# Optimization experiments

Measured on AMD Instinct MI355X. Metric: run time of the kernel, lower is better.

Reference implementation:

```python
import jax, jax.numpy as jnp
import numpy as np

# --- fixed module hyperparameters (from init_kwargs) ---
B, N, DIM = 1, 1024, 1024
HEADS, KV_HEADS, DH = 16, 4, 64
BS = 32                 # block_size
NUM_SEL = 8             # num_selected_blocks (< num blocks, so min() is NUM_SEL)
MEM = 1                 # num_compressed_mem_kv
W = N // BS             # num compress blocks (seq divisible by block -> no padding paths)
G = HEADS // KV_HEADS   # grouped queries per kv head
CDIM = BS * DH          # compress mlp input dim
HID = CDIM              # compress_mlp_expand_factor = 1.0
EPS = 1e-6


def setup_inputs() -> dict:
    key = jax.random.key(0)
    ks = jax.random.split(key, 12)
    s = 0.02
    f32 = jnp.float32
    return {
        "inp": jax.random.normal(ks[0], (B, N, DIM), f32),
        "g_norm": jnp.ones((DIM,), f32),                                   # RMSNorm weight
        "w_qkv": jax.random.normal(ks[1], (DIM, (HEADS + 2 * KV_HEADS) * DH), f32) * s,
        "mem_kv": jax.random.normal(ks[2], (2, KV_HEADS, MEM, DH), f32) * s,
        "k_pos": jax.random.normal(ks[3], (KV_HEADS, BS, DH), f32) * s,    # intra-block pos
        "v_pos": jax.random.normal(ks[4], (KV_HEADS, BS, DH), f32) * s,
        "k_w1": jax.random.normal(ks[5], (CDIM, HID), f32) * s,
        "k_b1": jnp.zeros((HID,), f32),
        "k_w2": jax.random.normal(ks[6], (HID, DH), f32) * s,
        "k_b2": jnp.zeros((DH,), f32),
        "v_w1": jax.random.normal(ks[7], (CDIM, HID), f32) * s,
        "v_b1": jnp.zeros((HID,), f32),
        "v_w2": jax.random.normal(ks[8], (HID, DH), f32) * s,
        "v_b2": jnp.zeros((DH,), f32),
        "gate_w": jax.random.normal(ks[9], (DIM, 2 * HEADS), f32) * s,
        "gate_b": jnp.full((2 * HEADS,), -2.0, f32),                       # bias init from source
        "w_out": jax.random.normal(ks[10], (HEADS * DH, DIM), f32) * s,
    }


def _rotary(x):
    # interleaved rotary (rotary-embedding-torch default), x: (b, h, n, d)
    n, d = x.shape[-2], x.shape[-1]
    inv_freq = 1.0 / (10000.0 ** (jnp.arange(0, d, 2, dtype=jnp.float32) / d))
    freqs = jnp.arange(n, dtype=jnp.float32)[:, None] * inv_freq            # (n, d/2)
    cos = jnp.repeat(jnp.cos(freqs), 2, axis=-1).astype(x.dtype)
    sin = jnp.repeat(jnp.sin(freqs), 2, axis=-1).astype(x.dtype)
    xr = jnp.stack([-x[..., 1::2], x[..., 0::2]], axis=-1).reshape(x.shape)  # rotate_half
    return x * cos + xr * sin


def reference(inp, g_norm, w_qkv, mem_kv, k_pos, v_pos,
              k_w1, k_b1, k_w2, k_b2, v_w1, v_b1, v_w2, v_b2,
              gate_w, gate_b, w_out):
    scale = DH ** -0.5
    # RMSNorm
    x = inp * jax.lax.rsqrt(jnp.mean(jnp.square(inp), -1, keepdims=True) + EPS) * g_norm
    qkv = x @ w_qkv
    q = qkv[..., : HEADS * DH].reshape(B, N, HEADS, DH).transpose(0, 2, 1, 3)
    k = qkv[..., HEADS * DH : (HEADS + KV_HEADS) * DH].reshape(B, N, KV_HEADS, DH).transpose(0, 2, 1, 3)
    v = qkv[..., (HEADS + KV_HEADS) * DH :].reshape(B, N, KV_HEADS, DH).transpose(0, 2, 1, 3)

    # --- compressed branch: MLP-pool each block of BS keys/values ---
    kpe = k + jnp.tile(k_pos, (1, W, 1))[None]               # (B,KV,N,DH)
    vpe = v + jnp.tile(v_pos, (1, W, 1))[None]
    ck = jax.nn.relu(kpe.reshape(B, KV_HEADS, W, CDIM) @ k_w1 + k_b1) @ k_w2 + k_b2   # (B,KV,W,DH)
    cv = jax.nn.relu(vpe.reshape(B, KV_HEADS, W, CDIM) @ v_w1 + v_b1) @ v_w2 + v_b2
    ck = jnp.concatenate([jnp.broadcast_to(mem_kv[0], (B, KV_HEADS, MEM, DH)), ck], axis=2)
    cv = jnp.concatenate([jnp.broadcast_to(mem_kv[1], (B, KV_HEADS, MEM, DH)), cv], axis=2)

    qg = q.reshape(B, KV_HEADS, G, N, DH)
    csim = jnp.einsum('bhgid,bhjd->bhgij', qg, ck) * scale   # (B,KV,G,N,MEM+W)
    cattn = jax.nn.softmax(csim, axis=-1)
    c_out = jnp.einsum('bhgij,bhjd->bhgid', cattn, cv).reshape(B, HEADS, N, DH)

    # rotary only for the fine branch (applied after compressed attention)
    q = _rotary(q)
    k = _rotary(k)

    # --- block selection from compressed similarities (query heads share) ---
    imp = csim[..., MEM:].mean(axis=2)                       # (B,KV,N,W)
    imp = jnp.pad(imp, ((0, 0), (0, 0), (0, 0), (1, 0)), constant_values=-1000.0)
    imp = jax.nn.softmax(imp, axis=-1)[..., 1:]
    sel_vals, sel_idx = jax.lax.top_k(imp, NUM_SEL)          # (B,KV,N,S)
    fmask = sel_vals > 1e-10

    # always include each query's own block (diagonal block), fully attended
    own = jnp.broadcast_to((jnp.arange(N) // BS)[None, None, :, None], (B, KV_HEADS, N, 1))
    sel_idx = jnp.concatenate([sel_idx, own], axis=-1)       # (B,KV,N,S+1)
    fmask = jnp.concatenate([fmask, jnp.ones(own.shape, bool)], axis=-1)

    # --- gather selected KV blocks per query position (irregular access) ---
    kb = k.reshape(B, KV_HEADS, W, BS, DH)
    vb = v.reshape(B, KV_HEADS, W, BS, DH)
    b_ix = jnp.arange(B)[:, None, None, None]
    h_ix = jnp.arange(KV_HEADS)[None, :, None, None]
    J = (NUM_SEL + 1) * BS
    fk = kb[b_ix, h_ix, sel_idx].reshape(B, KV_HEADS, N, J, DH)
    fv = vb[b_ix, h_ix, sel_idx].reshape(B, KV_HEADS, N, J, DH)
    fmask = jnp.repeat(fmask, BS, axis=-1)                   # (B,KV,N,J)

    fq = q.reshape(B, KV_HEADS, G, N, DH)
    fsim = jnp.einsum('bhgid,bhijd->bhgij', fq, fk) * scale  # (B,KV,G,N,J)
    fsim = jnp.where(fmask[:, :, None], fsim, -jnp.finfo(fsim.dtype).max)
    fattn = jax.nn.softmax(fsim, axis=-1)
    f_out = jnp.einsum('bhgij,bhijd->bhgid', fattn, fv).reshape(B, HEADS, N, DH)

    # --- learned sigmoid gating of the two branches ---
    gates = jax.nn.sigmoid(x @ gate_w + gate_b).reshape(B, N, HEADS, 2).transpose(0, 2, 1, 3)
    out = gates[..., 0:1] * c_out + gates[..., 1:2] * f_out  # (B,H,N,DH)
    out = out.transpose(0, 2, 1, 3).reshape(B, N, HEADS * DH)
    return out @ w_out
```

## Files before the change

### kernel.cpp

```cpp
#include <hip/hip_runtime.h>
#include <math.h>

#define NTOK 1024
#define DDIM 1024
#define HEADS 16
#define KVH 4
#define DH 64
#define BSZ 32
#define NSEL 8
#define WBLK 32
#define GQ 4
#define CDIM 2048
#define HIDN 2048
#define QKVD 1536
#define SCALE 0.125f
#define NEGINF (-__builtin_inff())

typedef unsigned short u16;
typedef u16   u16x8  __attribute__((ext_vector_type(8)));
typedef short short8 __attribute__((ext_vector_type(8)));
typedef float f32x4  __attribute__((ext_vector_type(4)));

__device__ __forceinline__ u16 f2bf(float f) {
    unsigned u = __float_as_uint(f);
    return (u16)((u + 0x7fffu + ((u >> 16) & 1u)) >> 16);
}
__device__ __forceinline__ float bf2f(u16 h) { return __uint_as_float(((unsigned)h) << 16); }

__device__ __forceinline__ void glds16(const void* g, void* l) {
    __builtin_amdgcn_global_load_lds(
        (const __attribute__((address_space(1))) unsigned int*)g,
        (__attribute__((address_space(3))) unsigned int*)l, 16, 0, 0);
}

__device__ __forceinline__ size_t tiled_off(int row, int k, int K) {
    return ((size_t)((row >> 4) * (K >> 5) + (k >> 5)) * 64 +
            ((row & 15) | (((k >> 3) & 3) << 4))) * 8;
}

__global__ void rmsnorm_kernel(const float* __restrict__ inp, const float* __restrict__ g,
                               u16* __restrict__ xhi, u16* __restrict__ xlo) {
    int t = threadIdx.x;
    int half = t >> 7, tid = t & 127;
    int n = blockIdx.x * 2 + half;
    const float4* row = (const float4*)(inp + (size_t)n * DDIM);
    float4 v0 = row[tid * 2], v1 = row[tid * 2 + 1];
    float ss = v0.x*v0.x + v0.y*v0.y + v0.z*v0.z + v0.w*v0.w
             + v1.x*v1.x + v1.y*v1.y + v1.z*v1.z + v1.w*v1.w;
    for (int off = 32; off; off >>= 1) ss += __shfl_down(ss, off);
    __shared__ float red[4];
    if ((t & 63) == 0) red[t >> 6] = ss;
    __syncthreads();
    float tot = red[half * 2] + red[half * 2 + 1];
    float r = 1.f / sqrtf(tot * (1.f / DDIM) + 1e-6f);
    const float4* gp = (const float4*)g;
    float4 g0 = gp[tid * 2], g1 = gp[tid * 2 + 1];
    float o[8] = { v0.x*r*g0.x, v0.y*r*g0.y, v0.z*r*g0.z, v0.w*r*g0.w,
                   v1.x*r*g1.x, v1.y*r*g1.y, v1.z*r*g1.z, v1.w*r*g1.w };
    u16x8 h, l;
#pragma unroll
    for (int i = 0; i < 8; ++i) {
        u16 hh = f2bf(o[i]);
        h[i] = hh;
        l[i] = f2bf(o[i] - bf2f(hh));
    }
    size_t ob = tiled_off(n, tid * 8, DDIM);
    *(u16x8*)&xhi[ob] = h;
    *(u16x8*)&xlo[ob] = l;
}

__global__ void transpose_split(const float* __restrict__ W, u16* __restrict__ Thi,
                                u16* __restrict__ Tlo, int K, int N) {
    __shared__ float tile[64][65];
    int k0 = blockIdx.y * 64, n0 = blockIdx.x * 64;
    int t = threadIdx.x;
    int r = t >> 4, c4 = (t & 15) * 4;
#pragma unroll
    for (int p = 0; p < 4; ++p) {
        float4 v = *(const float4*)&W[(size_t)(k0 + r + p * 16) * N + n0 + c4];
        tile[r + p * 16][c4 + 0] = v.x;
        tile[r + p * 16][c4 + 1] = v.y;
        tile[r + p * 16][c4 + 2] = v.z;
        tile[r + p * 16][c4 + 3] = v.w;
    }
    __syncthreads();
    int n = t >> 2, ks = (t & 3) * 16;
#pragma unroll
    for (int c = 0; c < 2; ++c) {
        u16x8 h, l;
#pragma unroll
        for (int j = 0; j < 8; ++j) {
            float v = tile[ks + c * 8 + j][n];
            u16 hh = f2bf(v);
            h[j] = hh;
            l[j] = f2bf(v - bf2f(hh));
        }
        size_t ob = tiled_off(n0 + n, k0 + ks + c * 8, K);
        *(u16x8*)&Thi[ob] = h;
        if (Tlo) *(u16x8*)&Tlo[ob] = l;
    }
}

__global__ void pad_small_tiled(const float* __restrict__ W, const float* __restrict__ b,
                                u16* __restrict__ Thi, u16* __restrict__ Tlo,
                                float* __restrict__ bias_pad, int K, int Xn, int KLOG) {
    int idx = blockIdx.x * 256 + threadIdx.x;
    int k = (idx & ((K >> 3) - 1)) * 8;
    int n = idx >> (KLOG - 3);
    if (n >= 128) return;
    u16x8 h, l;
#pragma unroll
    for (int j = 0; j < 8; ++j) {
        float v = (n < Xn) ? W[(size_t)(k + j) * Xn + n] : 0.f;
        u16 hh = f2bf(v);
        h[j] = hh;
        l[j] = f2bf(v - bf2f(hh));
    }
    size_t ob = tiled_off(n, k, K);
    *(u16x8*)&Thi[ob] = h;
    *(u16x8*)&Tlo[ob] = l;
    if (k == 0) bias_pad[n] = (n < Xn) ? b[n] : 0.f;
}

template<int SPLIT, int ACT, int FINAL>
__global__ __launch_bounds__(256, 1)
void gemm_tiled(const u16* __restrict__ Ahi0, const u16* __restrict__ Alo0,
                const u16* __restrict__ Bhi0, const u16* __restrict__ Blo0,
                const float* __restrict__ bias0, float* __restrict__ C0,
                const u16* __restrict__ Ahi1, const u16* __restrict__ Alo1,
                const u16* __restrict__ Bhi1, const u16* __restrict__ Blo1,
                const float* __restrict__ bias1, float* __restrict__ C1,
                int M, int N, int K, int S) {
    int batch = blockIdx.z / S;
    int s = blockIdx.z - batch * S;
    const u16* Ahi = batch ? Ahi1 : Ahi0;
    const u16* Alo = batch ? Alo1 : Alo0;
    const u16* Bhi = batch ? Bhi1 : Bhi0;
    const u16* Blo = batch ? Blo1 : Blo0;
    const float* bias = batch ? bias1 : bias0;
    float* C = batch ? C1 : C0;

    constexpr int PARTS = (SPLIT == 3) ? 2 : 1;
    __shared__ u16 smA[2 * PARTS * 8 * 512];
    __shared__ u16 smB[2 * PARTS * 8 * 512];

    int tid = threadIdx.x;
    int w = tid >> 6, L = tid & 63;
    int m15 = L & 15, q = L >> 4;
    int KT = K >> 5;
    int rowTile = blockIdx.y * 8, colTile = blockIdx.x * 8;
    int NIT = (K / S) >> 5;
    int kb0 = s * NIT;
    int aw = w & 1, bw = w >> 1;

    f32x4 acc[4][4];
#pragma unroll
    for (int i = 0; i < 4; ++i)
#pragma unroll
        for (int j = 0; j < 4; ++j) acc[i][j] = (f32x4){0.f, 0.f, 0.f, 0.f};

    auto stage = [&](int buf, int kb) {
#pragma unroll
        for (int rl = 0; rl < 2; ++rl) {
            int rb = 2 * w + rl;
            glds16(Ahi + ((size_t)(rowTile + rb) * KT + kb) * 512 + (size_t)L * 8,
                   &smA[((buf * PARTS + 0) * 8 + rb) * 512]);
            glds16(Bhi + ((size_t)(colTile + rb) * KT + kb) * 512 + (size_t)L * 8,
                   &smB[((buf * PARTS + 0) * 8 + rb) * 512]);
            if constexpr (SPLIT == 3) {
                glds16(Alo + ((size_t)(rowTile + rb) * KT + kb) * 512 + (size_t)L * 8,
                       &smA[((buf * PARTS + 1) * 8 + rb) * 512]);
                glds16(Blo + ((size_t)(colTile + rb) * KT + kb) * 512 + (size_t)L * 8,
                       &smB[((buf * PARTS + 1) * 8 + rb) * 512]);
            }
        }
    };

    stage(0, kb0);
    for (int it = 0; it < NIT; ++it) {
        __syncthreads();
        if (it + 1 < NIT) stage((it + 1) & 1, kb0 + it + 1);
        int buf = it & 1;
        short8 ah[4], bh[4];
#pragma unroll
        for (int i = 0; i < 4; ++i) {
            ah[i] = *(const short8*)&smA[((buf * PARTS + 0) * 8 + aw * 4 + i) * 512 + L * 8];
            bh[i] = *(const short8*)&smB[((buf * PARTS + 0) * 8 + bw * 4 + i) * 512 + L * 8];
        }
        if constexpr (SPLIT == 3) {
            short8 al[4], bl[4];
#pragma unroll
            for (int i = 0; i < 4; ++i) {
                al[i] = *(const short8*)&smA[((buf * PARTS + 1) * 8 + aw * 4 + i) * 512 + L * 8];
                bl[i] = *(const short8*)&smB[((buf * PARTS + 1) * 8 + bw * 4 + i) * 512 + L * 8];
            }
#pragma unroll
            for (int i = 0; i < 4; ++i)
#pragma unroll
                for (int j = 0; j < 4; ++j) {
                    acc[i][j] = __builtin_amdgcn_mfma_f32_16x16x32_bf16(ah[i], bl[j], acc[i][j], 0, 0, 0);
                    acc[i][j] = __builtin_amdgcn_mfma_f32_16x16x32_bf16(al[i], bh[j], acc[i][j], 0, 0, 0);
                    acc[i][j] = __builtin_amdgcn_mfma_f32_16x16x32_bf16(ah[i], bh[j], acc[i][j], 0, 0, 0);
                }
        } else {
#pragma unroll
            for (int i = 0; i < 4; ++i)
#pragma unroll
                for (int j = 0; j < 4; ++j)
                    acc[i][j] = __builtin_amdgcn_mfma_f32_16x16x32_bf16(ah[i], bh[j], acc[i][j], 0, 0, 0);
        }
    }

    if constexpr (FINAL == 0) C += (size_t)s * M * N;
#pragma unroll
    for (int i = 0; i < 4; ++i) {
        int row = rowTile * 16 + aw * 64 + i * 16 + q * 4;
#pragma unroll
        for (int j = 0; j < 4; ++j) {
            int col = colTile * 16 + bw * 64 + j * 16 + m15;
            float bv = (FINAL && bias) ? bias[col] : 0.f;
#pragma unroll
            for (int r = 0; r < 4; ++r) {
                float v = acc[i][j][r];
                if constexpr (FINAL) {
                    v += bv;
                    if (ACT == 1) v = fmaxf(v, 0.f);
                    if (ACT == 2) v = 1.f / (1.f + expf(-v));
                }
                C[(size_t)(row + r) * N + col] = v;
            }
        }
    }
}

template<int ACT>
__global__ void reduce_f32(const float* __restrict__ P0, const float* __restrict__ bias0,
                           float* __restrict__ C0,
                           const float* __restrict__ P1, const float* __restrict__ bias1,
                           float* __restrict__ C1, int S, int M, int N) {
    const float* P = blockIdx.y ? P1 : P0;
    const float* bias = blockIdx.y ? bias1 : bias0;
    float* C = blockIdx.y ? C1 : C0;
    int idx = blockIdx.x * 256 + threadIdx.x;
    int mn4 = (M * N) >> 2;
    if (idx >= mn4) return;
    f32x4 a = ((const f32x4*)P)[idx];
    for (int s = 1; s < S; ++s) a += ((const f32x4*)P)[(size_t)s * mn4 + idx];
    int col = (idx % (N >> 2)) * 4;
    f32x4 o;
#pragma unroll
    for (int j = 0; j < 4; ++j) {
        float v = a[j] + (bias ? bias[col + j] : 0.f);
        if (ACT == 1) v = fmaxf(v, 0.f);
        if (ACT == 2) v = 1.f / (1.f + expf(-v));
        o[j] = v;
    }
    ((f32x4*)C)[idx] = o;
}

__global__ void reduce_hid(const float* __restrict__ P0, const float* __restrict__ b0,
                           u16* __restrict__ hi0, u16* __restrict__ lo0,
                           const float* __restrict__ P1, const float* __restrict__ b1,
                           u16* __restrict__ hi1, u16* __restrict__ lo1, int S) {
    const float* P = blockIdx.y ? P1 : P0;
    const float* bias = blockIdx.y ? b1 : b0;
    u16* hi = blockIdx.y ? hi1 : hi0;
    u16* lo = blockIdx.y ? lo1 : lo0;
    int idx = blockIdx.x * 256 + threadIdx.x;
    int col = (idx & 255) * 8, rowi = idx >> 8;
    size_t base = ((size_t)rowi * HIDN + col) >> 2;
    f32x4 a0 = ((const f32x4*)P)[base], a1 = ((const f32x4*)P)[base + 1];
    for (int s = 1; s < S; ++s) {
        size_t sb = (size_t)s * (128 * HIDN / 4) + base;
        a0 += ((const f32x4*)P)[sb];
        a1 += ((const f32x4*)P)[sb + 1];
    }
    u16x8 h, l;
#pragma unroll
    for (int j = 0; j < 8; ++j) {
        float v = (j < 4 ? a0[j] : a1[j - 4]) + bias[col + j];
        v = fmaxf(v, 0.f);
        u16 hh = f2bf(v);
        h[j] = hh;
        l[j] = f2bf(v - bf2f(hh));
    }
    size_t ob = tiled_off(rowi, col, HIDN);
    *(u16x8*)&hi[ob] = h;
    *(u16x8*)&lo[ob] = l;
}

__global__ void reduce_ckcv(const float* __restrict__ Pk, const float* __restrict__ Pv,
                            const float* __restrict__ mem_kv,
                            const float* __restrict__ kb2, const float* __restrict__ vb2,
                            float* __restrict__ ck, float* __restrict__ cv, int S) {
    int idx = blockIdx.x * 256 + threadIdx.x;
    if (idx >= KVH * 33 * DH) return;
    int d = idx & 63;
    int j = (idx >> 6) % 33;
    int h = idx / (33 * 64);
    float kvv, vvv;
    if (j == 0) {
        kvv = mem_kv[(0 * KVH + h) * DH + d];
        vvv = mem_kv[(1 * KVH + h) * DH + d];
    } else {
        size_t base = (size_t)(h * WBLK + (j - 1)) * 128 + d;
        float ak = Pk[base], av = Pv[base];
        for (int s = 1; s < S; ++s) {
            ak += Pk[(size_t)s * (128 * 128) + base];
            av += Pv[(size_t)s * (128 * 128) + base];
        }
        kvv = ak + kb2[d];
        vvv = av + vb2[d];
    }
    ck[idx] = kvv;
    cv[idx] = vvv;
}

__global__ void build_cmlp_in(const float* __restrict__ qkv, const float* __restrict__ k_pos,
                              const float* __restrict__ v_pos,
                              u16* __restrict__ ckhi, u16* __restrict__ cklo,
                              u16* __restrict__ cvhi, u16* __restrict__ cvlo) {
    int idx = blockIdx.x * 256 + threadIdx.x;
    int k = (idx & 255) * 8;
    int r = idx >> 8;
    int p = k >> 6, d = k & 63;
    int h = r >> 5, wb = r & 31;
    int nn = wb * BSZ + p;
    const float* kq = qkv + (size_t)nn * QKVD + (HEADS + h) * DH + d;
    const float* vq = qkv + (size_t)nn * QKVD + (HEADS + KVH + h) * DH + d;
    const float* kp = k_pos + (size_t)(h * BSZ + p) * DH + d;
    const float* vp = v_pos + (size_t)(h * BSZ + p) * DH + d;
    u16x8 kh, kl, vh, vl;
#pragma unroll
    for (int j = 0; j < 8; ++j) {
        float kv = kq[j] + kp[j];
        float vv = vq[j] + vp[j];
        u16 a = f2bf(kv), b = f2bf(vv);
        kh[j] = a; kl[j] = f2bf(kv - bf2f(a));
        vh[j] = b; vl[j] = f2bf(vv - bf2f(b));
    }
    size_t ob = tiled_off(r, k, CDIM);
    *(u16x8*)&ckhi[ob] = kh; *(u16x8*)&cklo[ob] = kl;
    *(u16x8*)&cvhi[ob] = vh; *(u16x8*)&cvlo[ob] = vl;
}

__global__ void rotary_kernel(const float* __restrict__ qkv,
                              float* __restrict__ qr, float* __restrict__ kr,
                              float* __restrict__ vr) {
    int idx = blockIdx.x * 256 + threadIdx.x;
    int i = idx & 31;
    int n = (idx >> 5) & 1023;
    int hd = idx >> 15;
    if (hd >= 24) return;
    if (hd >= HEADS + KVH) {
        int h = hd - (HEADS + KVH);
        const float* src = qkv + (size_t)n * QKVD + (HEADS + KVH + h) * DH;
        float* dst = vr + ((size_t)h * NTOK + n) * DH;
        dst[2 * i] = src[2 * i];
        dst[2 * i + 1] = src[2 * i + 1];
        return;
    }
    float inv = powf(10000.f, -(float)i / 32.f);
    float fr = (float)n * inv;
    float c = cosf(fr), s = sinf(fr);
    const float* src; float* dst;
    if (hd < HEADS) { src = qkv + (size_t)n * QKVD + hd * DH;          dst = qr + ((size_t)hd * NTOK + n) * DH; }
    else { int h = hd - HEADS;
           src = qkv + (size_t)n * QKVD + (HEADS + h) * DH;            dst = kr + ((size_t)h * NTOK + n) * DH; }
    float x0 = src[2 * i], x1 = src[2 * i + 1];
    dst[2 * i]     = x0 * c - x1 * s;
    dst[2 * i + 1] = x1 * c + x0 * s;
}

__global__ __launch_bounds__(256)
void cattn_kernel(const float* __restrict__ qkv, const float* __restrict__ ck,
                  const float* __restrict__ cv, float* __restrict__ c_out,
                  int* __restrict__ sel, int* __restrict__ selmask) {
    int h = blockIdx.y;
    int tid = threadIdx.x;
    int w = tid >> 6, lane = tid & 63;
    int grp = lane >> 4, sub = lane & 15;
    int n = blockIdx.x * 4 + w;
    __shared__ float cks[33 * 68];
    __shared__ float cvs[33 * 68];
    __shared__ float sims[16 * 36];

    for (int t4 = tid; t4 < 1056; t4 += 256) {
        int half = (t4 >= 528) ? 1 : 0;
        int u = t4 - half * 528;
        int j = u >> 4, d4 = (u & 15) * 4;
        const float* src = (half ? cv : ck) + (size_t)h * 33 * 64 + j * 64 + d4;
        float* dst = (half ? cvs : cks) + j * 68 + d4;
        *(float4*)dst = *(const float4*)src;
    }
    float qreg[64];
    {
        const float4* qp4 = (const float4*)(qkv + (size_t)n * QKVD + (h * GQ + grp) * DH);
#pragma unroll
        for (int c = 0; c < 16; ++c) {
            float4 v = qp4[c];
            qreg[4 * c] = v.x; qreg[4 * c + 1] = v.y; qreg[4 * c + 2] = v.z; qreg[4 * c + 3] = v.w;
        }
    }
    __syncthreads();

#pragma unroll
    for (int r = 0; r < 3; ++r) {
        int j = r * 16 + sub;
        if (j < 33) {
            float acc = 0.f;
#pragma unroll
            for (int d = 0; d < 64; ++d) acc = fmaf(qreg[d], cks[j * 68 + d], acc);
            sims[(w * 4 + grp) * 36 + j] = acc * SCALE;
        }
    }

    float ival = NEGINF;
    if (lane < 32)
        ival = 0.25f * (sims[(w * 4 + 0) * 36 + 1 + lane] + sims[(w * 4 + 1) * 36 + 1 + lane] +
                        sims[(w * 4 + 2) * 36 + 1 + lane] + sims[(w * 4 + 3) * 36 + 1 + lane]);
    float m = ival;
    for (int off = 32; off; off >>= 1) m = fmaxf(m, __shfl_xor(m, off));
    float e = (lane < 32) ? expf(ival - m) : 0.f;
    float sum = e;
    for (int off = 32; off; off >>= 1) sum += __shfl_xor(sum, off);
    float p = (lane < 32) ? e / sum : NEGINF;

    float v = p;
    int base = (h * NTOK + n) * 9;
    for (int t = 0; t < NSEL; ++t) {
        float bv = v; int bi = lane;
        for (int off = 32; off; off >>= 1) {
            float ov = __shfl_xor(bv, off);
            int   oi = __shfl_xor(bi, off);
            if (ov > bv || (ov == bv && oi < bi)) { bv = ov; bi = oi; }
        }
        if (lane == 0) { sel[base + t] = bi; selmask[base + t] = (bv > 1e-10f) ? 1 : 0; }
        if (lane == bi) v = NEGINF;
    }
    if (lane == 0) { sel[base + NSEL] = n >> 5; selmask[base + NSEL] = 1; }

#pragma unroll
    for (int g = 0; g < 4; ++g) {
        float sv = (lane < 33) ? sims[(w * 4 + g) * 36 + lane] : NEGINF;
        float mm = sv;
        for (int off = 32; off; off >>= 1) mm = fmaxf(mm, __shfl_xor(mm, off));
        float ee = (lane < 33) ? __expf(sv - mm) : 0.f;
        float ssum = ee;
        for (int off = 32; off; off >>= 1) ssum += __shfl_xor(ssum, off);
        if (lane < 33) sims[(w * 4 + g) * 36 + lane] = ee / ssum;
    }

    f32x4 o = (f32x4){0.f, 0.f, 0.f, 0.f};
#pragma unroll
    for (int j = 0; j < 33; ++j) {
        float a = sims[(w * 4 + grp) * 36 + j];
        f32x4 vv = *(const f32x4*)&cvs[j * 68 + sub * 4];
        o += a * vv;
    }
    *(f32x4*)&c_out[(((size_t)(h * GQ + grp)) * NTOK + n) * DH + sub * 4] = o;
}

__global__ void fattn_kernel(const float* __restrict__ qr, const float* __restrict__ kr,
                             const float* __restrict__ vr, const int* __restrict__ sel,
                             const int* __restrict__ selmask, float* __restrict__ f_out) {
    int n = blockIdx.x, h = blockIdx.y;
    int tid = threadIdx.x;
    int w = tid >> 6, lane = tid & 63;
    int grp = lane >> 4, sub = lane & 15;
    __shared__ float qsm[4 * 68];
    __shared__ float KV[64 * 64];
    __shared__ float ps[4 * 68];
    __shared__ float msm[16], lsm[16];
    __shared__ int sel_s[9], msk_s[9];

    if (tid < 9) {
        sel_s[tid] = sel[(h * NTOK + n) * 9 + tid];
        msk_s[tid] = selmask[(h * NTOK + n) * 9 + tid];
    }
    qsm[w * 68 + lane] = qr[(((size_t)(h * GQ + w)) * NTOK + n) * DH + lane];
    f32x4 o4 = (f32x4){0.f, 0.f, 0.f, 0.f};
    float m_run = -3.402823466e38f, l_run = 0.f;
    __syncthreads();

    const float* krh_ = kr + (size_t)h * NTOK * DH;
    const float* vrh_ = vr + (size_t)h * NTOK * DH;

    int rl = lane >> 4, sl = lane & 15;

    auto stageRows = [&](const float* src, int bp) {
        int nrow = (bp < 4) ? 64 : 32;
        if (w * 16 < nrow) {
            int myblk = sel_s[bp * 2 + (w >> 1)];
            const float* b_ = src + (size_t)myblk * BSZ * DH;
#pragma unroll
            for (int cc = 0; cc < 4; ++cc) {
                int r = w * 16 + cc * 4 + rl;
                int sg = sl ^ (r & 15);
                glds16(b_ + (size_t)(r & 31) * DH + sg * 4, &KV[(w * 16 + cc * 4) * 64]);
            }
        }
    };

    stageRows(krh_, 0);

    for (int bp = 0; bp < 5; ++bp) {
        int nrow = (bp < 4) ? 64 : 32;

        asm volatile("s_waitcnt vmcnt(0)" ::: "memory");
        __builtin_amdgcn_sched_barrier(0);

        float s = -3.402823466e38f;
        {
            int jj = w * 16 + sub;
            int b = bp * 2 + (jj >> 5);
            if (jj < nrow && msk_s[b]) {
                int sw = jj & 15;
                const float* Kb = &KV[jj * 64];
                float acc = 0.f;
#pragma unroll
                for (int c = 0; c < 16; ++c) {
                    f32x4 k4 = *(const f32x4*)&Kb[(c ^ sw) * 4];
                    f32x4 q4 = *(const f32x4*)&qsm[grp * 68 + c * 4];
                    acc = fmaf(q4[0], k4[0], acc);
                    acc = fmaf(q4[1], k4[1], acc);
                    acc = fmaf(q4[2], k4[2], acc);
                    acc = fmaf(q4[3], k4[3], acc);
                }
                s = acc * SCALE;
            }
        }
        float mb = s;
        for (int off = 8; off; off >>= 1) mb = fmaxf(mb, __shfl_xor(mb, off));
        float m_new = fmaxf(m_run, mb);
        float pp = (s > -1e37f) ? __expf(s - m_new) : 0.f;
        float alpha = __expf(m_run - m_new);
        float psum = pp;
        for (int off = 8; off; off >>= 1) psum += __shfl_xor(psum, off);
        l_run = l_run * alpha + psum;
        m_run = m_new;
        ps[w * 68 + grp * 16 + sub] = pp;

        __builtin_amdgcn_sched_barrier(0);
        asm volatile("s_waitcnt lgkmcnt(0)" ::: "memory");
        __builtin_amdgcn_sched_barrier(0);
        stageRows(vrh_, bp);

        asm volatile("s_waitcnt vmcnt(0)" ::: "memory");
        __builtin_amdgcn_sched_barrier(0);

        o4 *= alpha;
        {
            int jbase = w * 16;
            if (jbase < nrow) {
#pragma unroll
                for (int jq = 0; jq < 4; ++jq) {
                    f32x4 p4 = *(const f32x4*)&ps[w * 68 + grp * 16 + jq * 4];
#pragma unroll
                    for (int r = 0; r < 4; ++r) {
                        int row = jbase + jq * 4 + r;
                        int slot = sub ^ (row & 15);
                        f32x4 vv = *(const f32x4*)&KV[row * 64 + slot * 4];
                        o4 += p4[r] * vv;
                    }
                }
            }
        }
        if (bp < 4) {
            __builtin_amdgcn_sched_barrier(0);
            asm volatile("s_waitcnt lgkmcnt(0)" ::: "memory");
            __builtin_amdgcn_sched_barrier(0);
            stageRows(krh_, bp + 1);
        }
    }
    if (sub == 0) { msm[w * 4 + grp] = m_run; lsm[w * 4 + grp] = l_run; }
    __syncthreads();
    *(f32x4*)&KV[(w * 4 + grp) * 64 + sub * 4] = o4;
    __syncthreads();
    float m0 = msm[0 * 4 + w], m1 = msm[1 * 4 + w], m2 = msm[2 * 4 + w], m3 = msm[3 * 4 + w];
    float M = fmaxf(fmaxf(m0, m1), fmaxf(m2, m3));
    float f0 = __expf(m0 - M), f1 = __expf(m1 - M), f2 = __expf(m2 - M), f3 = __expf(m3 - M);
    float L = lsm[0 * 4 + w] * f0 + lsm[1 * 4 + w] * f1 + lsm[2 * 4 + w] * f2 + lsm[3 * 4 + w] * f3;
    float sum = KV[(0 * 4 + w) * 64 + lane] * f0 + KV[(1 * 4 + w) * 64 + lane] * f1
              + KV[(2 * 4 + w) * 64 + lane] * f2 + KV[(3 * 4 + w) * 64 + lane] * f3;
    f_out[(((size_t)(h * GQ + w)) * NTOK + n) * DH + lane] = sum / L;
}

__global__ void mix_kernel(const float* __restrict__ gates, const float* __restrict__ c_out,
                           const float* __restrict__ f_out,
                           u16* __restrict__ mixhi, u16* __restrict__ mixlo) {
    int idx = blockIdx.x * 256 + threadIdx.x;
    int col = (idx & 127) * 8;
    int n = idx >> 7;
    int hd = col >> 6, d = col & 63;
    float g0 = gates[(size_t)n * 128 + hd * 2];
    float g1 = gates[(size_t)n * 128 + hd * 2 + 1];
    size_t hoff = (((size_t)hd) * NTOK + n) * DH + d;
    u16x8 h, l;
#pragma unroll
    for (int j = 0; j < 8; ++j) {
        float v = g0 * c_out[hoff + j] + g1 * f_out[hoff + j];
        u16 hh = f2bf(v);
        h[j] = hh;
        l[j] = f2bf(v - bf2f(hh));
    }
    size_t ob = tiled_off(n, col, DDIM);
    *(u16x8*)&mixhi[ob] = h;
    *(u16x8*)&mixlo[ob] = l;
}

extern "C" void kernel_launch(void* const* d_in, const int* in_sizes, int n_in,
                              void* d_out, int out_size, void* d_ws, size_t ws_size,
                              hipStream_t stream) {
    const float* inp    = (const float*)d_in[0];
    const float* g_norm = (const float*)d_in[1];
    const float* w_qkv  = (const float*)d_in[2];
    const float* mem_kv = (const float*)d_in[3];
    const float* k_pos  = (const float*)d_in[4];
    const float* v_pos  = (const float*)d_in[5];
    const float* k_w1   = (const float*)d_in[6];
    const float* k_b1   = (const float*)d_in[7];
    const float* k_w2   = (const float*)d_in[8];
    const float* k_b2   = (const float*)d_in[9];
    const float* v_w1   = (const float*)d_in[10];
    const float* v_b1   = (const float*)d_in[11];
    const float* v_w2   = (const float*)d_in[12];
    const float* v_b2   = (const float*)d_in[13];
    const float* gate_w = (const float*)d_in[14];
    const float* gate_b = (const float*)d_in[15];
    const float* w_out  = (const float*)d_in[16];
    float* out = (float*)d_out;

    char* wsb = (char*)d_ws;
    size_t off = 0;
    auto alloc = [&](size_t bytes) -> void* {
        void* p = wsb + off;
        off = (off + bytes + 255) & ~(size_t)255;
        return p;
    };
    u16*   xhi    = (u16*)  alloc((size_t)NTOK * DDIM * 2);
    u16*   xlo    = (u16*)  alloc((size_t)NTOK * DDIM * 2);
    float* qkvb   = (float*)alloc((size_t)NTOK * QKVD * 4);
    u16*   wqThi  = (u16*)  alloc((size_t)QKVD * DDIM * 2);
    u16*   wqTlo  = (u16*)  alloc((size_t)QKVD * DDIM * 2);
    u16*   kw1Thi = (u16*)  alloc((size_t)HIDN * CDIM * 2);
    u16*   kw1Tlo = (u16*)  alloc((size_t)HIDN * CDIM * 2);
    u16*   vw1Thi = (u16*)  alloc((size_t)HIDN * CDIM * 2);
    u16*   vw1Tlo = (u16*)  alloc((size_t)HIDN * CDIM * 2);
    u16*   woThi  = (u16*)  alloc((size_t)DDIM * DDIM * 2);
    u16*   gwThi  = (u16*)  alloc((size_t)128 * DDIM * 2);
    u16*   gwTlo  = (u16*)  alloc((size_t)128 * DDIM * 2);
    float* gbp    = (float*)alloc(128 * 4);
    u16*   kw2Thi = (u16*)  alloc((size_t)128 * HIDN * 2);
    u16*   kw2Tlo = (u16*)  alloc((size_t)128 * HIDN * 2);
    float* kb2p   = (float*)alloc(128 * 4);
    u16*   vw2Thi = (u16*)  alloc((size_t)128 * HIDN * 2);
    u16*   vw2Tlo = (u16*)  alloc((size_t)128 * HIDN * 2);
    float* vb2p   = (float*)alloc(128 * 4);
    u16*   cinkhi = (u16*)  alloc((size_t)128 * CDIM * 2);
    u16*   cinklo = (u16*)  alloc((size_t)128 * CDIM * 2);
    u16*   cinvhi = (u16*)  alloc((size_t)128 * CDIM * 2);
    u16*   cinvlo = (u16*)  alloc((size_t)128 * CDIM * 2);
    u16*   hidkhi = (u16*)  alloc((size_t)128 * HIDN * 2);
    u16*   hidklo = (u16*)  alloc((size_t)128 * HIDN * 2);
    u16*   hidvhi = (u16*)  alloc((size_t)128 * HIDN * 2);
    u16*   hidvlo = (u16*)  alloc((size_t)128 * HIDN * 2);
    float* Pg     = (float*)alloc((size_t)8 * NTOK * 128 * 4);
    float* Pm1k   = (float*)alloc((size_t)4 * 128 * HIDN * 4);
    float* Pm1v   = (float*)alloc((size_t)4 * 128 * HIDN * 4);
    float* Pm2k   = (float*)alloc((size_t)8 * 128 * 128 * 4);
    float* Pm2v   = (float*)alloc((size_t)8 * 128 * 128 * 4);
    float* ck     = (float*)alloc((size_t)KVH * 33 * DH * 4);
    float* cv     = (float*)alloc((size_t)KVH * 33 * DH * 4);
    float* qr     = (float*)alloc((size_t)HEADS * NTOK * DH * 4);
    float* kr     = (float*)alloc((size_t)KVH * NTOK * DH * 4);
    float* vr     = (float*)alloc((size_t)KVH * NTOK * DH * 4);
    float* c_out  = (float*)alloc((size_t)HEADS * NTOK * DH * 4);
    float* f_out  = (float*)alloc((size_t)HEADS * NTOK * DH * 4);
    float* gates  = (float*)alloc((size_t)NTOK * 128 * 4);
    int*   sel    = (int*)  alloc((size_t)KVH * NTOK * 9 * 4);
    int*   selmask= (int*)  alloc((size_t)KVH * NTOK * 9 * 4);
    u16*   mixhi  = (u16*)  alloc((size_t)NTOK * DDIM * 2);
    u16*   mixlo  = (u16*)  alloc((size_t)NTOK * DDIM * 2);

    transpose_split<<<dim3(QKVD / 64, DDIM / 64), 256, 0, stream>>>(w_qkv, wqThi, wqTlo, DDIM, QKVD);
    transpose_split<<<dim3(HIDN / 64, CDIM / 64), 256, 0, stream>>>(k_w1, kw1Thi, kw1Tlo, CDIM, HIDN);
    transpose_split<<<dim3(HIDN / 64, CDIM / 64), 256, 0, stream>>>(v_w1, vw1Thi, vw1Tlo, CDIM, HIDN);
    transpose_split<<<dim3(DDIM / 64, DDIM / 64), 256, 0, stream>>>(w_out, woThi, nullptr, DDIM, DDIM);
    pad_small_tiled<<<(128 * DDIM / 8) / 256, 256, 0, stream>>>(gate_w, gate_b, gwThi, gwTlo, gbp, DDIM, 32, 10);
    pad_small_tiled<<<(128 * HIDN / 8) / 256, 256, 0, stream>>>(k_w2, k_b2, kw2Thi, kw2Tlo, kb2p, HIDN, 64, 11);
    pad_small_tiled<<<(128 * HIDN / 8) / 256, 256, 0, stream>>>(v_w2, v_b2, vw2Thi, vw2Tlo, vb2p, HIDN, 64, 11);

    rmsnorm_kernel<<<NTOK / 2, 256, 0, stream>>>(inp, g_norm, xhi, xlo);
    gemm_tiled<3, 0, 1><<<dim3(QKVD / 128, NTOK / 128, 1), 256, 0, stream>>>(
        xhi, xlo, wqThi, wqTlo, nullptr, qkvb,
        xhi, xlo, wqThi, wqTlo, nullptr, qkvb, NTOK, QKVD, DDIM, 1);
    gemm_tiled<3, 0, 0><<<dim3(1, NTOK / 128, 8), 256, 0, stream>>>(
        xhi, xlo, gwThi, gwTlo, nullptr, Pg,
        xhi, xlo, gwThi, gwTlo, nullptr, Pg, NTOK, 128, DDIM, 8);
    reduce_f32<2><<<dim3(128, 1), 256, 0, stream>>>(Pg, gbp, gates, Pg, gbp, gates, 8, NTOK, 128);
    build_cmlp_in<<<128, 256, 0, stream>>>(qkvb, k_pos, v_pos, cinkhi, cinklo, cinvhi, cinvlo);
    gemm_tiled<3, 0, 0><<<dim3(HIDN / 128, 1, 8), 256, 0, stream>>>(
        cinkhi, cinklo, kw1Thi, kw1Tlo, nullptr, Pm1k,
        cinvhi, cinvlo, vw1Thi, vw1Tlo, nullptr, Pm1v, 128, HIDN, CDIM, 4);
    reduce_hid<<<dim3(128, 2), 256, 0, stream>>>(Pm1k, k_b1, hidkhi, hidklo,
                                                 Pm1v, v_b1, hidvhi, hidvlo, 4);
    gemm_tiled<3, 0, 0><<<dim3(1, 1, 16), 256, 0, stream>>>(
        hidkhi, hidklo, kw2Thi, kw2Tlo, nullptr, Pm2k,
        hidvhi, hidvlo, vw2Thi, vw2Tlo, nullptr, Pm2v, 128, 128, HIDN, 8);
    reduce_ckcv<<<33, 256, 0, stream>>>(Pm2k, Pm2v, mem_kv, kb2p, vb2p, ck, cv, 8);
    rotary_kernel<<<(24 * NTOK * 32) / 256, 256, 0, stream>>>(qkvb, qr, kr, vr);
    cattn_kernel<<<dim3(NTOK / 4, KVH), 256, 0, stream>>>(qkvb, ck, cv, c_out, sel, selmask);
    fattn_kernel<<<dim3(NTOK, KVH), 256, 0, stream>>>(qr, kr, vr, sel, selmask, f_out);
    mix_kernel<<<(NTOK * DDIM / 8) / 256, 256, 0, stream>>>(gates, c_out, f_out, mixhi, mixlo);
    gemm_tiled<1, 0, 1><<<dim3(DDIM / 128, NTOK / 128, 1), 256, 0, stream>>>(
        mixhi, mixhi, woThi, woThi, nullptr, out,
        mixhi, mixhi, woThi, woThi, nullptr, out, NTOK, DDIM, DDIM, 1);
}
```

Before: 346.7 us.

## Split K/V shared buffers in fine attention to overlap prefetch with compute

The fine-attention kernel now keeps separate shared buffers for K and V instead of one reused buffer. The next K block is prefetched while V for the current block is consumed, with partial vmcnt waits replacing full drains. The QK dot products and PV accumulation also use split accumulators for more instruction-level parallelism. This doubles the shared-memory footprint of that buffer, and the counter-based waits depend on exact counts of outstanding loads.

```diff
diff --git a/kernel.cpp b/kernel.cpp
--- a/kernel.cpp
+++ b/kernel.cpp
@@ -469,7 +469,8 @@
     int w = tid >> 6, lane = tid & 63;
     int grp = lane >> 4, sub = lane & 15;
     __shared__ float qsm[4 * 68];
-    __shared__ float KV[64 * 64];
+    __shared__ float Ksm[64 * 64];
+    __shared__ float Vsm[64 * 64];
     __shared__ float ps[4 * 68];
     __shared__ float msm[16], lsm[16];
     __shared__ int sel_s[9], msk_s[9];
@@ -488,7 +489,7 @@
 
     int rl = lane >> 4, sl = lane & 15;
 
-    auto stageRows = [&](const float* src, int bp) {
+    auto stageRows = [&](float* dstbuf, const float* src, int bp) {
         int nrow = (bp < 4) ? 64 : 32;
         if (w * 16 < nrow) {
             int myblk = sel_s[bp * 2 + (w >> 1)];
@@ -497,17 +498,18 @@
             for (int cc = 0; cc < 4; ++cc) {
                 int r = w * 16 + cc * 4 + rl;
                 int sg = sl ^ (r & 15);
-                glds16(b_ + (size_t)(r & 31) * DH + sg * 4, &KV[(w * 16 + cc * 4) * 64]);
+                glds16(b_ + (size_t)(r & 31) * DH + sg * 4, &dstbuf[(w * 16 + cc * 4) * 64]);
             }
         }
     };
 
-    stageRows(krh_, 0);
+    stageRows(Ksm, krh_, 0);
+    stageRows(Vsm, vrh_, 0);
 
     for (int bp = 0; bp < 5; ++bp) {
         int nrow = (bp < 4) ? 64 : 32;
 
-        asm volatile("s_waitcnt vmcnt(0)" ::: "memory");
+        asm volatile("s_waitcnt vmcnt(4)" ::: "memory");
         __builtin_amdgcn_sched_barrier(0);
 
         float s = -3.402823466e38f;
@@ -516,18 +518,20 @@
             int b = bp * 2 + (jj >> 5);
             if (jj < nrow && msk_s[b]) {
                 int sw = jj & 15;
-                const float* Kb = &KV[jj * 64];
-                float acc = 0.f;
-#pragma unroll
-                for (int c = 0; c < 16; ++c) {
-                    f32x4 k4 = *(const f32x4*)&Kb[(c ^ sw) * 4];
-                    f32x4 q4 = *(const f32x4*)&qsm[grp * 68 + c * 4];
-                    acc = fmaf(q4[0], k4[0], acc);
-                    acc = fmaf(q4[1], k4[1], acc);
-                    acc = fmaf(q4[2], k4[2], acc);
-                    acc = fmaf(q4[3], k4[3], acc);
+                const float* Kb = &Ksm[jj * 64];
+                f32x4 a0 = (f32x4){0.f, 0.f, 0.f, 0.f};
+                f32x4 a1 = (f32x4){0.f, 0.f, 0.f, 0.f};
+#pragma unroll
+                for (int c = 0; c < 16; c += 2) {
+                    f32x4 k4a = *(const f32x4*)&Kb[(c ^ sw) * 4];
+                    f32x4 q4a = *(const f32x4*)&qsm[grp * 68 + c * 4];
+                    f32x4 k4b = *(const f32x4*)&Kb[((c + 1) ^ sw) * 4];
+                    f32x4 q4b = *(const f32x4*)&qsm[grp * 68 + (c + 1) * 4];
+                    a0 += q4a * k4a;
+                    a1 += q4b * k4b;
                 }
-                s = acc * SCALE;
+                f32x4 at = a0 + a1;
+                s = ((at[0] + at[1]) + (at[2] + at[3])) * SCALE;
             }
         }
         float mb = s;
@@ -544,13 +548,17 @@
         __builtin_amdgcn_sched_barrier(0);
         asm volatile("s_waitcnt lgkmcnt(0)" ::: "memory");
         __builtin_amdgcn_sched_barrier(0);
-        stageRows(vrh_, bp);
-
-        asm volatile("s_waitcnt vmcnt(0)" ::: "memory");
+        if (bp < 4) {
+            stageRows(Ksm, krh_, bp + 1);
+            asm volatile("s_waitcnt vmcnt(4)" ::: "memory");
+        } else {
+            asm volatile("s_waitcnt vmcnt(0)" ::: "memory");
+        }
         __builtin_amdgcn_sched_barrier(0);
 
-        o4 *= alpha;
         {
+            f32x4 t0 = (f32x4){0.f, 0.f, 0.f, 0.f};
+            f32x4 t1 = (f32x4){0.f, 0.f, 0.f, 0.f};
             int jbase = w * 16;
             if (jbase < nrow) {
 #pragma unroll
@@ -560,29 +568,31 @@
                     for (int r = 0; r < 4; ++r) {
                         int row = jbase + jq * 4 + r;
                         int slot = sub ^ (row & 15);
-                        f32x4 vv = *(const f32x4*)&KV[row * 64 + slot * 4];
-                        o4 += p4[r] * vv;
+                        f32x4 vv = *(const f32x4*)&Vsm[row * 64 + slot * 4];
+                        if (r & 1) t1 += p4[r] * vv;
+                        else       t0 += p4[r] * vv;
                     }
                 }
             }
+            o4 = o4 * alpha + (t0 + t1);
         }
         if (bp < 4) {
             __builtin_amdgcn_sched_barrier(0);
             asm volatile("s_waitcnt lgkmcnt(0)" ::: "memory");
             __builtin_amdgcn_sched_barrier(0);
-            stageRows(krh_, bp + 1);
+            stageRows(Vsm, vrh_, bp + 1);
         }
     }
     if (sub == 0) { msm[w * 4 + grp] = m_run; lsm[w * 4 + grp] = l_run; }
     __syncthreads();
-    *(f32x4*)&KV[(w * 4 + grp) * 64 + sub * 4] = o4;
+    *(f32x4*)&Ksm[(w * 4 + grp) * 64 + sub * 4] = o4;
     __syncthreads();
     float m0 = msm[0 * 4 + w], m1 = msm[1 * 4 + w], m2 = msm[2 * 4 + w], m3 = msm[3 * 4 + w];
     float M = fmaxf(fmaxf(m0, m1), fmaxf(m2, m3));
     float f0 = __expf(m0 - M), f1 = __expf(m1 - M), f2 = __expf(m2 - M), f3 = __expf(m3 - M);
     float L = lsm[0 * 4 + w] * f0 + lsm[1 * 4 + w] * f1 + lsm[2 * 4 + w] * f2 + lsm[3 * 4 + w] * f3;
-    float sum = KV[(0 * 4 + w) * 64 + lane] * f0 + KV[(1 * 4 + w) * 64 + lane] * f1
-              + KV[(2 * 4 + w) * 64 + lane] * f2 + KV[(3 * 4 + w) * 64 + lane] * f3;
+    float sum = Ksm[(0 * 4 + w) * 64 + lane] * f0 + Ksm[(1 * 4 + w) * 64 + lane] * f1
+              + Ksm[(2 * 4 + w) * 64 + lane] * f2 + Ksm[(3 * 4 + w) * 64 + lane] * f3;
     f_out[(((size_t)(h * GQ + w)) * NTOK + n) * DH + lane] = sum / L;
 }
 
```

Result: no change. 345.3 us (-0.4%).
